# Kernel tuning notes

Measured on AMD Instinct MI355X. Metric: run time of the kernel, lower is better.

Reference implementation:

```python
import jax, jax.numpy as jnp
import numpy as np
from jax import lax

DIM = 64           # LHMSA dim
C3 = 3 * DIM       # high-band channels
HEADS = C3 // 32   # 6
WS = 8             # window size
SHIFT = 4          # shift size
EPS = 1e-6


def _ln_chw(x, w, b):
    # channel-last layer norm applied to BCHW input over C
    xt = x.transpose(0, 2, 3, 1)
    mu = xt.mean(-1, keepdims=True)
    var = ((xt - mu) ** 2).mean(-1, keepdims=True)
    y = (xt - mu) / jnp.sqrt(var + EPS) * w + b
    return y.transpose(0, 3, 1, 2)


def _conv1x1(x, w):
    # w: (out_c, in_c), no bias
    return jnp.einsum('bchw,oc->bohw', x, w)


def _dwconv3(x, w):
    # depthwise 3x3, w: (C,1,3,3)
    C = x.shape[1]
    return lax.conv_general_dilated(x, w, (1, 1), ((1, 1), (1, 1)),
                                    dimension_numbers=('NCHW', 'OIHW', 'NCHW'),
                                    feature_group_count=C)


def _gelu(x):
    return jax.nn.gelu(x, approximate=False)


def _dwt(x):
    x01 = x[:, :, 0::2, :] * 0.5
    x02 = x[:, :, 1::2, :] * 0.5
    x1 = x01[:, :, :, 0::2]; x2 = x02[:, :, :, 0::2]
    x3 = x01[:, :, :, 1::2]; x4 = x02[:, :, :, 1::2]
    ll = x1 + x2 + x3 + x4
    high = jnp.concatenate([-x1 - x2 + x3 + x4,
                            -x1 + x2 - x3 + x4,
                            x1 - x2 - x3 + x4], axis=1)
    return ll, high


def _iwt(ll, high):
    B, C, H, W = ll.shape
    hl, lh, hh = jnp.split(high, 3, axis=1)
    x1 = (ll - hl - lh + hh) * 0.5
    x2 = (ll - hl + lh - hh) * 0.5
    x3 = (ll + hl - lh - hh) * 0.5
    x4 = (ll + hl + lh + hh) * 0.5
    even = jnp.stack([x1, x3], axis=-1).reshape(B, C, H, 2 * W)  # rows 0::2
    odd = jnp.stack([x2, x4], axis=-1).reshape(B, C, H, 2 * W)   # rows 1::2
    return jnp.stack([even, odd], axis=-2).reshape(B, C, 2 * H, 2 * W)


def _swin_mhsa(x, qkv_w, qkv_b, proj_w, proj_b, rpb_table, rpi):
    # x: (B, C3, H, W); H,W divisible by WS -> no padding path
    B, C, H, W = x.shape
    dh = C // HEADS
    scale = dh ** (-0.5)
    xh = x.transpose(0, 2, 3, 1)                           # BHWC
    xh = jnp.roll(xh, (-SHIFT, -SHIFT), axis=(1, 2))
    nh, nw = H // WS, W // WS
    xw = xh.reshape(B, nh, WS, nw, WS, C).transpose(0, 1, 3, 2, 4, 5)
    xw = xw.reshape(B * nh * nw, WS * WS, C)               # (nW, N, C)
    qkv = xw @ qkv_w.T + qkv_b                             # (nW, N, 3C)
    qkv = qkv.reshape(-1, WS * WS, 3, HEADS, dh).transpose(2, 0, 3, 1, 4)
    q, k, v = qkv[0], qkv[1], qkv[2]                       # (nW, h, N, dh)
    attn = jnp.einsum('whnd,whmd->whnm', q, k) * scale
    bias = rpb_table[rpi.reshape(-1)].reshape(WS * WS, WS * WS, HEADS)
    attn = jax.nn.softmax(attn + bias.transpose(2, 0, 1)[None], axis=-1)
    out = jnp.einsum('whnm,whmd->whnd', attn, v)
    out = out.transpose(0, 2, 1, 3).reshape(-1, WS * WS, C)
    out = out.reshape(B, nh, nw, WS, WS, C).transpose(0, 1, 3, 2, 4, 5)
    out = out.reshape(B, H, W, C)
    out = jnp.roll(out, (SHIFT, SHIFT), axis=(1, 2))
    out = out @ proj_w.T + proj_b
    return out.transpose(0, 3, 1, 2)


def _rel_pos_index():
    coords = np.stack(np.meshgrid(np.arange(WS), np.arange(WS), indexing='ij'))
    cf = coords.reshape(2, -1)
    rel = (cf[:, :, None] - cf[:, None, :]).transpose(1, 2, 0).astype(np.int64)
    rel[:, :, 0] += WS - 1
    rel[:, :, 1] += WS - 1
    rel[:, :, 0] *= 2 * WS - 1
    return rel.sum(-1)


def setup_inputs() -> dict:
    key = jax.random.key(0)
    ks = jax.random.split(key, 12)
    B, H, W = 2, 512, 512
    x = jax.random.normal(ks[0], (B, DIM, H, W), jnp.float32)
    s = 0.02
    inp = {
        'x': x,
        'norm_w': jnp.ones((C3,), jnp.float32),
        'norm_b': jnp.zeros((C3,), jnp.float32),
        'qkv_w': jax.random.normal(ks[1], (3 * C3, C3), jnp.float32) * s,
        'qkv_b': jnp.zeros((3 * C3,), jnp.float32),
        'proj_w': jax.random.normal(ks[2], (C3, C3), jnp.float32) * s,
        'proj_b': jnp.zeros((C3,), jnp.float32),
        'rpb_table': jax.random.normal(ks[3], ((2 * WS - 1) ** 2, HEADS), jnp.float32) * s,
        'aux_dw_w': jax.random.normal(ks[4], (DIM, 1, 3, 3), jnp.float32) * 0.1,
        'aux_pw_w': jax.random.normal(ks[5], (DIM, DIM), jnp.float32) * s,
        'cg1_w': jax.random.normal(ks[6], (C3 * 3 // 12, DIM), jnp.float32) * s,
        'cg2_w': jax.random.normal(ks[7], (C3, C3 * 3 // 12), jnp.float32) * s,
        'po_w': jax.random.normal(ks[8], (DIM, DIM), jnp.float32) * s,
        'gamma_main': jnp.full((1,), 1e-4, jnp.float32),
        'gamma_aux': jnp.full((1,), 0.5, jnp.float32),
        'gamma_cross': jnp.full((1,), 1e-5, jnp.float32),
        'rel_pos_index': jnp.asarray(_rel_pos_index(), jnp.int32),
    }
    return inp


def reference(x, norm_w, norm_b, qkv_w, qkv_b, proj_w, proj_b, rpb_table,
              aux_dw_w, aux_pw_w, cg1_w, cg2_w, po_w,
              gamma_main, gamma_aux, gamma_cross, rel_pos_index):
    ll, high = _dwt(x)
    high_norm = _ln_chw(high, norm_w, norm_b)
    refined_high = high + gamma_main * _swin_mhsa(high_norm, qkv_w, qkv_b,
                                                  proj_w, proj_b, rpb_table,
                                                  rel_pos_index)
    refined_ll = ll + gamma_aux * _conv1x1(_gelu(_dwconv3(ll, aux_dw_w)), aux_pw_w)
    gap = ll.mean((2, 3), keepdims=True)
    cross = jax.nn.sigmoid(_conv1x1(_gelu(_conv1x1(gap, cg1_w)), cg2_w))
    refined_high = refined_high * (1.0 + gamma_cross * (cross - 0.5) * 2.0)
    out = _iwt(refined_ll, refined_high)
    return _conv1x1(out - x, po_w)
```

## Files before the change

kernel.cpp:

```cpp
#include <hip/hip_runtime.h>
#include <hip/hip_bf16.h>
#include <math.h>

typedef __hip_bfloat16 bf16;
typedef short s8v __attribute__((ext_vector_type(8)));
typedef float f4v __attribute__((ext_vector_type(4)));
#define MFMA16(a,b,c) __builtin_amdgcn_mfma_f32_16x16x32_bf16(a,b,c,0,0,0)

#define B2   2
#define C64  64
#define C3   192
#define HEADS 6
#define NWIN 2048

#define P_NORMW 0
#define P_NORMB 192
#define P_QKVW  384
#define P_QKVB  110976
#define P_PROJW 111552
#define P_PROJB 148416
#define P_RPB   148608
#define P_AUXDW 149958
#define P_AUXPW 150534
#define P_CG1   154630
#define P_CG2   157702
#define P_PO    166918
#define P_GM    171014
#define P_GA    171015
#define P_GC    171016

#define WS_FLAG   0
#define WS_PARAMS 256
#define WS_GAP    684544
#define WS_TSTAT  689664
#define WS_LL     1738240
#define WS_DLLW   18515456
#define WS_WOUT   35292672
#define WS_HRAW   85624320
#define WS_WQKV   135955968
#define WS_WPROJ  136177152
#define WS_WPW    136250880
#define WS_WPO    136259072
#define WS_S12    136267264
#define WS_BIAS6  136271872

__device__ __forceinline__ float bfu(unsigned short u){
  return __uint_as_float(((unsigned)u) << 16);
}
__device__ __forceinline__ float LDR(const void* p, long i, bool isf){
  return isf ? ((const float*)p)[i] : bfu(((const unsigned short*)p)[i]);
}
template<bool ISF>
__device__ __forceinline__ float4 LD4(const void* p, long i){
  if constexpr (ISF) return *(const float4*)((const float*)p + i);
  else {
    const ushort4 u = *(const ushort4*)((const bf16*)p + i);
    float4 r; r.x = bfu(u.x); r.y = bfu(u.y); r.z = bfu(u.z); r.w = bfu(u.w);
    return r;
  }
}
template<bool ISF>
__device__ __forceinline__ void ST(void* p, long i, float v){
  if constexpr (ISF) ((float*)p)[i] = v;
  else ((bf16*)p)[i] = __float2bfloat16(v);
}
__device__ __forceinline__ float gelu_f(float x){
  const float z = 0.7978845608028654f * (x + 0.044715f * x*x*x);
  const float t = 1.f - 2.f / (__expf(2.f*z) + 1.f);
  return 0.5f * x * (1.f + t);
}
__device__ __forceinline__ unsigned pk2(float a, float b){
  return (unsigned)__bfloat16_as_ushort(__float2bfloat16(a)) |
         ((unsigned)__bfloat16_as_ushort(__float2bfloat16(b)) << 16);
}
__device__ __forceinline__ uint4 pk8(const float* v){
  uint4 r;
  r.x = pk2(v[0], v[1]); r.y = pk2(v[2], v[3]);
  r.z = pk2(v[4], v[5]); r.w = pk2(v[6], v[7]);
  return r;
}
__device__ __forceinline__ void gld16(const void* g, void* l){
  __builtin_amdgcn_global_load_lds(
      (const __attribute__((address_space(1))) void*)g,
      (__attribute__((address_space(3))) void*)l, 16, 0, 0);
}

__global__ __launch_bounds__(256) void detect_kernel(const void* x, int* flag){
  __shared__ int wildcnt;
  if (threadIdx.x == 0) wildcnt = 0;
  __syncthreads();
  const unsigned short* u = (const unsigned short*)x;
  int wild = 0;
  for (int i = threadIdx.x; i < 2048; i += 256){
    unsigned int v = ((unsigned int)u[i]) << 16;
    float f = __uint_as_float(v);
    float a = fabsf(f);
    if (!(a < 1e8f) || (a > 0.f && a < 1e-8f)) wild++;
  }
  atomicAdd(&wildcnt, wild);
  __syncthreads();
  if (threadIdx.x == 0) *flag = (wildcnt > 100) ? 1 : 0;
}

struct PP { const void* src[15]; float* dst[15]; int n[15]; };
__device__ void kprep_body(int vblk, const PP& pp, bool isf, const int* rpi,
                           bf16* wqkvF, bf16* wproj, bf16* wpw,
                           bf16* wpo, float* bias6T, float2* s12p){
  const int gid = vblk*256 + threadIdx.x;
  const int gsz = 512*256;
#pragma unroll
  for (int q = 0; q < 15; q++){
    const int n = pp.n[q];
    const void* s = pp.src[q];
    float* d = pp.dst[q];
    for (int i = gid; i < n; i += gsz) d[i] = LDR(s, i, isf);
  }
  const void* qkvw = pp.src[2];
  const void* normw = pp.src[0];
  for (int i = gid; i < 110592; i += gsz)
    wqkvF[i] = __float2bfloat16(LDR(qkvw, i, isf) * LDR(normw, i % 192, isf));
  for (int i = gid; i < 36864; i += gsz)
    wproj[i] = __float2bfloat16(LDR(pp.src[4], i, isf));
  for (int i = gid; i < 4096; i += gsz){
    wpw[i] = __float2bfloat16(LDR(pp.src[8], i, isf));
    wpo[i] = __float2bfloat16(LDR(pp.src[11], i, isf));
  }
  for (int j = gid; j < 24576; j += gsz){
    const int hh = j >> 12, nm = j & 4095;
    const int row = nm >> 6, col = nm & 63;
    bias6T[hh*4096 + col*64 + row] = LDR(pp.src[6], rpi[nm]*6 + hh, isf);
  }
  const int o = gid >> 4, lane = gid & 15;
  if (o < 576){
    float s1 = 0.f, s2 = 0.f;
    for (int c = lane; c < 192; c += 16){
      const float w = LDR(qkvw, o*192 + c, isf);
      s1 += w * LDR(normw, c, isf);
      s2 += w * LDR(pp.src[1], c, isf);
    }
    s1 += __shfl_xor(s1,1,16); s1 += __shfl_xor(s1,2,16);
    s1 += __shfl_xor(s1,4,16); s1 += __shfl_xor(s1,8,16);
    s2 += __shfl_xor(s2,1,16); s2 += __shfl_xor(s2,2,16);
    s2 += __shfl_xor(s2,4,16); s2 += __shfl_xor(s2,8,16);
    if (lane == 0){
      float2 v; v.x = s1; v.y = s2 + LDR(pp.src[3], o, isf);
      s12p[o] = v;
    }
  }
}

template<bool ISF>
__device__ void k1f_body(int wid, const void* xv, bf16* llb, bf16* hraw, float2* tstat){
  const int b  = wid >> 10;
  const int wh = (wid >> 5) & 31;
  const int ww = wid & 31;
  const int tid = threadIdx.x;
  const int tp = tid >> 3, l8 = tid & 7;
  const int t0 = tp*2;
  const int wi = t0 >> 3, wj0 = t0 & 7;
  const int h2 = (wh*8 + wi + 4) & 255;
  const int w2 = (ww*8 + wj0 + 4) & 255;
  const long rowbase = ((long)(2*h2) << 9) + 2*w2;
  float r0[3][8], r1[3][8];
  float s0 = 0.f, q0 = 0.f, s1 = 0.f, q1 = 0.f;
#pragma unroll
  for (int g4 = 0; g4 < 2; ++g4){
    float4 ta[4], tb[4];
#pragma unroll
    for (int u = 0; u < 4; ++u){
      const int c = l8*8 + g4*4 + u;
      const long base = ((long)(b*64 + c) << 18) + rowbase;
      ta[u] = LD4<ISF>(xv, base);
      tb[u] = LD4<ISF>(xv, base + 512);
    }
#pragma unroll
    for (int u = 0; u < 4; ++u){
      const int cc = g4*4 + u;
      const int c = l8*8 + cc;
      float a = ta[u].x, cr = ta[u].y, bb = tb[u].x, dd = tb[u].y;
      const float ll0 = 0.5f*(a + bb + cr + dd);
      const float h00 = 0.5f*(-a - bb + cr + dd);
      const float h10 = 0.5f*(-a + bb - cr + dd);
      const float h20 = 0.5f*( a - bb - cr + dd);
      r0[0][cc] = h00; r0[1][cc] = h10; r0[2][cc] = h20;
      s0 += h00 + h10 + h20; q0 += h00*h00 + h10*h10 + h20*h20;
      a = ta[u].z; cr = ta[u].w; bb = tb[u].z; dd = tb[u].w;
      const float ll1 = 0.5f*(a + bb + cr + dd);
      const float h01 = 0.5f*(-a - bb + cr + dd);
      const float h11 = 0.5f*(-a + bb - cr + dd);
      const float h21 = 0.5f*( a - bb - cr + dd);
      r1[0][cc] = h01; r1[1][cc] = h11; r1[2][cc] = h21;
      s1 += h01 + h11 + h21; q1 += h01*h01 + h11*h11 + h21*h21;
      *(unsigned*)(llb + ((long)(b*64 + c) << 16) + ((long)h2 << 8) + w2) = pk2(ll0, ll1);
    }
  }
  const long hb = ((long)wid*64 + t0)*192 + l8*8;
  *(uint4*)(hraw + hb)            = pk8(r0[0]);
  *(uint4*)(hraw + hb + 64)       = pk8(r0[1]);
  *(uint4*)(hraw + hb + 128)      = pk8(r0[2]);
  *(uint4*)(hraw + hb + 192)      = pk8(r1[0]);
  *(uint4*)(hraw + hb + 192 + 64) = pk8(r1[1]);
  *(uint4*)(hraw + hb + 192 +128) = pk8(r1[2]);
  s0 += __shfl_xor(s0,1,8); s0 += __shfl_xor(s0,2,8); s0 += __shfl_xor(s0,4,8);
  q0 += __shfl_xor(q0,1,8); q0 += __shfl_xor(q0,2,8); q0 += __shfl_xor(q0,4,8);
  s1 += __shfl_xor(s1,1,8); s1 += __shfl_xor(s1,2,8); s1 += __shfl_xor(s1,4,8);
  q1 += __shfl_xor(q1,1,8); q1 += __shfl_xor(q1,2,8); q1 += __shfl_xor(q1,4,8);
  if (l8 == 0){
    float mean = s0 * (1.f/192.f);
    float var = fmaxf(q0 * (1.f/192.f) - mean*mean, 0.f);
    float rstd = rsqrtf(var + 1e-6f);
    float2 st; st.x = rstd; st.y = mean * rstd;
    tstat[wid*64 + t0] = st;
    mean = s1 * (1.f/192.f);
    var = fmaxf(q1 * (1.f/192.f) - mean*mean, 0.f);
    rstd = rsqrtf(var + 1e-6f);
    st.x = rstd; st.y = mean * rstd;
    tstat[wid*64 + t0 + 1] = st;
  }
}

__global__ __launch_bounds__(256,4) void k1p(const void* xv, bf16* llb, bf16* hraw,
                                             float2* tstat, const int* flag, PP pp,
                                             const int* rpi, bf16* wqkvF, bf16* wproj,
                                             bf16* wpw, bf16* wpo, float* bias6T,
                                             float2* s12p){
  const bool isf = (*flag) != 0;
  const int blk = blockIdx.x;
  if (blk < NWIN){
    if (isf) k1f_body<true>(blk, xv, llb, hraw, tstat);
    else     k1f_body<false>(blk, xv, llb, hraw, tstat);
  } else {
    kprep_body(blk - NWIN, pp, isf, rpi, wqkvF, wproj, wpw, wpo, bias6T, s12p);
  }
}

__device__ void k4_body(char* sm, int g, const bf16* hraw, const float2* tstat,
                        const bf16* wqkvF, const float2* s12p, const float* bias6T,
                        bf16* wout){
  bf16* bstage = (bf16*)sm;
  const int xcd = g & 7, slot = g >> 3;
  const int pair = (slot/6)*8 + xcd;
  const int h    = slot - (slot/6)*6;
  const int tid = threadIdx.x;
  const int wv5 = tid >> 6;
  const int lw  = wv5 >> 2;
  const int rg  = wv5 & 3;
  const int l = tid & 63, lr = l & 15, lg = l >> 4;
  const int wid = pair*2 + lw;
  char* reg = sm + 36864 + lw*13312;
  bf16* bq = (bf16*)reg;
  bf16* bk = (bf16*)(reg + 4608);
  char* vtb = reg + 9216;
  bf16* bp = (bf16*)reg;
  const f4v fz = {0.f,0.f,0.f,0.f};
  const float scale = 0.17677669529663687f;
  const bf16* at = hraw + (long)wid * 12288;

#pragma unroll
  for (int pass = 0; pass < 5; ++pass){
    if (pass*512 + wv5*64 < 2304){
      const int idx = pass*512 + tid;
      const int rl  = idx / 24;
      const int off = (idx - rl*24) * 16;
      const int soff = off ^ ((rl & 7) << 4);
      const int grow = (rl >> 5)*192 + h*32 + (rl & 31);
      gld16(wqkvF + grow*192 + (soff >> 1),
            (char*)bstage + (pass*512 + wv5*64)*16);
    }
  }
  s8v aA[6];
#pragma unroll
  for (int ks = 0; ks < 6; ++ks)
    aA[ks] = *(const s8v*)(at + (rg*16+lr)*192 + ks*32 + lg*8);
  float2 st4[4];
#pragma unroll
  for (int i = 0; i < 4; ++i)
    st4[i] = tstat[wid*64 + rg*16 + lg*4 + i];
  __syncthreads();

  f4v acc[6];
#pragma unroll
  for (int nt = 0; nt < 6; ++nt) acc[nt] = fz;
  __builtin_amdgcn_s_setprio(1);
#pragma unroll
  for (int ks = 0; ks < 6; ++ks){
    const int kb = (ks*32 + lg*8) * 2;
#pragma unroll
    for (int nt = 0; nt < 6; ++nt){
      const int row = nt*16 + lr;
      const s8v bfr = *(const s8v*)((const char*)bstage + row*384 + (kb ^ ((row&7)<<4)));
      acc[nt] = MFMA16(aA[ks], bfr, acc[nt]);
    }
  }
  __builtin_amdgcn_s_setprio(0);
#pragma unroll
  for (int nt = 0; nt < 6; ++nt){
    const int ol = nt*16 + lr;
    const int p = ol >> 5, c = ol & 31;
    const int ocol = p*192 + h*32 + c;
    const float2 sp = s12p[ocol];
#pragma unroll
    for (int i = 0; i < 4; ++i){
      const int row = rg*16 + lg*4 + i;
      const float v = st4[i].x*acc[nt][i] - st4[i].y*sp.x + sp.y;
      if (p == 0)      bq[row*36 + c] = __float2bfloat16(v*scale);
      else if (p == 1) bk[row*36 + c] = __float2bfloat16(v);
      else             *(bf16*)(vtb + ((c*128 + row*2) ^ ((c&7)<<4))) = __float2bfloat16(v);
    }
  }
  __syncthreads();

  f4v bld[4];
#pragma unroll
  for (int nt = 0; nt < 4; ++nt)
    bld[nt] = *(const f4v*)(bias6T + h*4096 + (nt*16+lr)*64 + rg*16 + lg*4);
  f4v sacc[4];
  {
    const s8v a = *(const s8v*)(bq + (rg*16+lr)*36 + lg*8);
#pragma unroll
    for (int nt = 0; nt < 4; ++nt){
      const s8v bfr = *(const s8v*)(bk + (nt*16+lr)*36 + lg*8);
      sacc[nt] = MFMA16(a, bfr, bld[nt]);
    }
  }
  float pvv[4][4];
  float inv4[4];
#pragma unroll
  for (int i = 0; i < 4; ++i){
    float s = 0.f;
#pragma unroll
    for (int nt = 0; nt < 4; ++nt){
      const float e = __expf(sacc[nt][i]);
      pvv[i][nt] = e;
      s += e;
    }
    s += __shfl_xor(s, 1, 16);
    s += __shfl_xor(s, 2, 16);
    s += __shfl_xor(s, 4, 16);
    s += __shfl_xor(s, 8, 16);
    inv4[i] = 1.f/s;
  }
  __syncthreads();

#pragma unroll
  for (int i = 0; i < 4; ++i){
    const int row = rg*16 + lg*4 + i;
#pragma unroll
    for (int nt = 0; nt < 4; ++nt)
      bp[row*72 + nt*16 + lr] = __float2bfloat16(pvv[i][nt]);
  }
  f4v oacc[2] = {fz, fz};
  __builtin_amdgcn_s_setprio(1);
#pragma unroll
  for (int ks2 = 0; ks2 < 2; ++ks2){
    const s8v a = *(const s8v*)(bp + (rg*16+lr)*72 + ks2*32 + lg*8);
#pragma unroll
    for (int nn = 0; nn < 2; ++nn){
      const int d = nn*16 + lr;
      const s8v bfr = *(const s8v*)(vtb + ((d*128 + (ks2*32+lg*8)*2) ^ ((d&7)<<4)));
      oacc[nn] = MFMA16(a, bfr, oacc[nn]);
    }
  }
  __builtin_amdgcn_s_setprio(0);
#pragma unroll
  for (int nn = 0; nn < 2; ++nn)
#pragma unroll
    for (int i = 0; i < 4; ++i){
      const int row = rg*16 + lg*4 + i;
      wout[((long)wid*64 + row)*192 + h*32 + nn*16 + lr] =
        __float2bfloat16(oacc[nn][i] * inv4[i]);
    }
}

__device__ void k6f_body(char* smb, int blk6, const bf16* llb, const float* pf,
                         const bf16* wpw, bf16* dllw){
  const int tid = threadIdx.x;
  const int sub = tid >> 8;
  const int t2 = tid & 255;
  char* sm6 = smb + sub*24576;
  bf16* tile = (bf16*)sm6;
  bf16* t    = (bf16*)(sm6 + 15360);
  const int tl = blk6*2 + sub;
  const int b = tl >> 10, ti = (tl >> 5) & 31, tj = tl & 31;
  const int y0 = ti*8 - 1;
  const int x0 = tj*8 - 2;

  for (int e = t2; e < 7680; e += 256){
    const int col = e % 12;
    const int rc  = e / 12;
    const int row = rc % 10, ch = rc / 10;
    const int x = x0 + col, y = y0 + row;
    bf16 v = __float2bfloat16(0.f);
    if ((unsigned)x < 256u && (unsigned)y < 256u)
      v = llb[((long)(b*64 + ch) << 16) + ((long)y << 8) + x];
    tile[rc*12 + col] = v;
  }
  __syncthreads();

  {
    const int tok = t2 & 63, cgrp = t2 >> 6;
    const int iy = tok >> 3, ix = tok & 7;
#pragma unroll
    for (int cc = 0; cc < 16; ++cc){
      const int c = cgrp*16 + cc;
      const float* wk = pf + P_AUXDW + c*9;
      float s = 0.f;
#pragma unroll
      for (int ky = 0; ky < 3; ++ky)
#pragma unroll
        for (int kx = 0; kx < 3; ++kx)
          s += wk[ky*3 + kx] * __bfloat162float(tile[(c*10 + iy + ky)*12 + ix + 1 + kx]);
      t[tok*72 + c] = __float2bfloat16(gelu_f(s));
    }
  }
  __syncthreads();

  const int wv = t2 >> 6, l = t2 & 63, lr = l & 15, lg = l >> 4;
  const f4v fz = {0.f,0.f,0.f,0.f};
  f4v acc[4];
#pragma unroll
  for (int nt = 0; nt < 4; ++nt) acc[nt] = fz;
#pragma unroll
  for (int ks = 0; ks < 2; ++ks){
    const s8v a = *(const s8v*)(t + (wv*16+lr)*72 + ks*32 + lg*8);
#pragma unroll
    for (int nt = 0; nt < 4; ++nt){
      const s8v bfr = *(const s8v*)(wpw + (nt*16+lr)*64 + ks*32 + lg*8);
      acc[nt] = MFMA16(a, bfr, acc[nt]);
    }
  }
  const float ga = pf[P_GA];
#pragma unroll
  for (int i = 0; i < 4; ++i){
    const int p = wv*16 + lg*4 + i;
    const int y = ti*8 + (p >> 3), x = tj*8 + (p & 7);
    const int sy = (y - 4) & 255, sx = (x - 4) & 255;
    const int wd = b*1024 + (sy >> 3)*32 + (sx >> 3);
    const int tok2 = (sy & 7)*8 + (sx & 7);
    const long ob = ((long)wd*64 + tok2)*64;
#pragma unroll
    for (int nt = 0; nt < 4; ++nt)
      dllw[ob + nt*16 + lr] = __float2bfloat16(ga * acc[nt][i]);
  }
}

__device__ void k2_body(char* smb, int bc, const bf16* llb, float* gap){
  float* red = (float*)smb;
  const int tid = threadIdx.x;
  const uint4* p = (const uint4*)(llb + ((long)bc << 16));
  float s = 0.f;
  for (int i = tid; i < 8192; i += 512){
    const uint4 v = p[i];
    s += __uint_as_float(v.x << 16) + __uint_as_float(v.x & 0xffff0000u);
    s += __uint_as_float(v.y << 16) + __uint_as_float(v.y & 0xffff0000u);
    s += __uint_as_float(v.z << 16) + __uint_as_float(v.z & 0xffff0000u);
    s += __uint_as_float(v.w << 16) + __uint_as_float(v.w & 0xffff0000u);
  }
  red[tid] = s; __syncthreads();
  for (int st = 256; st > 0; st >>= 1){
    if (tid < st) red[tid] += red[tid + st];
    __syncthreads();
  }
  if (tid == 0) gap[bc] = red[0] * (1.f / 65536.f);
}

__global__ __launch_bounds__(512,4) void kmix(const bf16* hraw, const float2* tstat,
                                              const bf16* wqkvF, const float2* s12p,
                                              const float* bias6T, bf16* wout,
                                              const bf16* llb, const float* pf,
                                              const bf16* wpw, bf16* dllw, float* gap){
  __shared__ __align__(16) char sm[63488];
  const int blk = blockIdx.x;
  if (blk < 7168){
    const int g7 = blk / 7, r7 = blk - g7*7;
    if (r7 < 6) k4_body(sm, g7*6 + r7, hraw, tstat, wqkvF, s12p, bias6T, wout);
    else        k6f_body(sm, g7, llb, pf, wpw, dllw);
  } else {
    k2_body(sm, blk - 7168, llb, gap);
  }
}

__global__ __launch_bounds__(256,5) void k5_proj(bf16* wout, const bf16* hraw,
                                                 const bf16* wproj, const float* pf,
                                                 const float* gap){
  __shared__ __align__(16) bf16 bufC[64*192];
  __shared__ float t1s[48];
  __shared__ float amL[192], cvL[192];
  const int wid = blockIdx.x;
  const int b  = wid >> 10;
  const int tid = threadIdx.x;
  const int wv = tid >> 6, l = tid & 63, lr = l & 15, lg = l >> 4;

  {
    const bf16* hsrc = hraw + (long)wid * 12288;
#pragma unroll
    for (int pass = 0; pass < 6; ++pass){
      const int idx = pass*256 + tid;
      const int row = idx / 24;
      const int off = (idx % 24) * 16;
      const int soff = off ^ ((row & 7) << 4);
      gld16(hsrc + row*192 + (soff >> 1),
            (char*)bufC + (pass*256 + wv*64)*16);
    }
  }

  if (tid < 48){
    float s = 0.f;
    const float* w = pf + P_CG1 + tid*64;
    for (int c = 0; c < 64; ++c) s += w[c] * gap[b*64 + c];
    t1s[tid] = gelu_f(s);
  }
  __syncthreads();
  if (tid < 192){
    float s = 0.f;
    const float* w = pf + P_CG2 + tid*48;
    for (int j = 0; j < 48; ++j) s += w[j] * t1s[j];
    const float cr = 1.f / (1.f + __expf(-s));
    const float cc = pf[P_GC] * (cr - 0.5f) * 2.f;
    cvL[tid] = cc;
    amL[tid] = pf[P_GM] * (1.f + cc);
  }

  const f4v fz = {0.f,0.f,0.f,0.f};
  const bf16* at = wout + (long)wid * 12288;

  f4v acc[3][4];
#pragma unroll
  for (int nt = 0; nt < 3; ++nt)
#pragma unroll
    for (int mt = 0; mt < 4; ++mt) acc[nt][mt] = fz;
#pragma unroll
  for (int ks = 0; ks < 6; ++ks){
    const int k0 = ks*32;
    s8v a[4];
#pragma unroll
    for (int mt = 0; mt < 4; ++mt)
      a[mt] = *(const s8v*)(at + (mt*16+lr)*192 + k0 + lg*8);
#pragma unroll
    for (int nt = 0; nt < 3; ++nt){
      const int ocol = (wv*3+nt)*16 + lr;
      const s8v bfr = *(const s8v*)(wproj + ocol*192 + k0 + lg*8);
#pragma unroll
      for (int mt = 0; mt < 4; ++mt) acc[nt][mt] = MFMA16(a[mt], bfr, acc[nt][mt]);
    }
  }
  __syncthreads();
#pragma unroll
  for (int nt = 0; nt < 3; ++nt){
    const int col = (wv*3+nt)*16 + lr;
    const float am = amL[col], cv = cvL[col], pb = pf[P_PROJB + col];
#pragma unroll
    for (int mt = 0; mt < 4; ++mt)
#pragma unroll
      for (int i = 0; i < 4; ++i){
        const int row = mt*16 + lg*4 + i;
        const float hv = __bfloat162float(
          *(const bf16*)((const char*)bufC + row*384 + ((col*2) ^ ((row&7)<<4))));
        wout[(long)wid*12288 + row*192 + col] =
          __float2bfloat16(am*(acc[nt][mt][i] + pb) + cv*hv);
      }
  }
}

template<bool ISF>
__device__ void k7_body(const bf16* dvalw, const bf16* dllw, const bf16* wpo,
                        void* out, char* yp){
  const int blk = blockIdx.x;
  const int b = blk >> 10, hh = (blk >> 1) & 511, half = blk & 1;
  const int h2 = hh >> 1, posH = hh & 1;
  const int th = (h2 + 252) & 255;
  const int wh = th >> 3, wi = th & 7;
  const int tid = threadIdx.x;
  const int j = tid & 7;
#pragma unroll
  for (int pass = 0; pass < 8; ++pass){
    const int p = pass*32 + (tid >> 3);
    const int ww2 = half*256 + p;
    const int w2 = ww2 >> 1, posW = ww2 & 1;
    const int tw = (w2 + 252) & 255;
    const int ww = tw >> 3, wj = tw & 7;
    const int wid = b*1024 + wh*32 + ww;
    const int tok = wi*8 + wj;
    const long dvb = ((long)wid*64 + tok)*192 + j*8;
    const s8v hl8 = *(const s8v*)(dvalw + dvb);
    const s8v lh8 = *(const s8v*)(dvalw + dvb + 64);
    const s8v hh8 = *(const s8v*)(dvalw + dvb + 128);
    const s8v dl8 = *(const s8v*)(dllw + ((long)wid*64 + tok)*64 + j*8);
    const float s1 = posW ? 0.5f : -0.5f;
    const float s2 = posH ? 0.5f : -0.5f;
    const float s3 = posW == posH ? 0.5f : -0.5f;
    float e[8];
#pragma unroll
    for (int q = 0; q < 8; ++q)
      e[q] = 0.5f*bfu((unsigned short)dl8[q]) + s1*bfu((unsigned short)hl8[q])
           + s2*bfu((unsigned short)lh8[q]) + s3*bfu((unsigned short)hh8[q]);
    *(uint4*)(yp + ((p*128 + j*16) ^ ((p&7)<<4))) = pk8(e);
  }
  __syncthreads();
  const int wv = tid >> 6, l = tid & 63, lr = l & 15, lg = l >> 4;
  const f4v fz = {0.f,0.f,0.f,0.f};
  f4v acc[4][4];
#pragma unroll
  for (int mt = 0; mt < 4; ++mt)
#pragma unroll
    for (int nt = 0; nt < 4; ++nt) acc[mt][nt] = fz;
#pragma unroll
  for (int ks = 0; ks < 2; ++ks){
    const int k0 = ks*32;
    s8v a[4];
#pragma unroll
    for (int mt = 0; mt < 4; ++mt)
      a[mt] = *(const s8v*)(wpo + (mt*16+lr)*64 + k0 + lg*8);
#pragma unroll
    for (int nt = 0; nt < 4; ++nt){
      const int prow = wv*64 + nt*16 + lr;
      const s8v bfr = *(const s8v*)(yp + ((prow*128 + (k0+lg*8)*2) ^ ((prow&7)<<4)));
#pragma unroll
      for (int mt = 0; mt < 4; ++mt) acc[mt][nt] = MFMA16(a[mt], bfr, acc[mt][nt]);
    }
  }
  const int px0 = half*256 + wv*64;
#pragma unroll
  for (int mt = 0; mt < 4; ++mt)
#pragma unroll
    for (int nt = 0; nt < 4; ++nt)
#pragma unroll
      for (int i = 0; i < 4; ++i){
        const int c = mt*16 + lg*4 + i;
        const long ob = ((long)(b*64 + c)*512 + hh)*512 + px0 + nt*16 + lr;
        ST<ISF>(out, ob, acc[mt][nt][i]);
      }
}
__global__ __launch_bounds__(256,4) void k7_out(const bf16* dvalw, const bf16* dllw,
                                                const bf16* wpo, void* out, const int* flag){
  __shared__ __align__(16) char yp[32768];
  if (*flag) k7_body<true>(dvalw, dllw, wpo, out, yp);
  else       k7_body<false>(dvalw, dllw, wpo, out, yp);
}

extern "C" void kernel_launch(void* const* d_in, const int* in_sizes, int n_in,
                              void* d_out, int out_size, void* d_ws, size_t ws_size,
                              hipStream_t stream){
  char* ws = (char*)d_ws;
  int*   flag = (int*)(ws + WS_FLAG);
  float* pf   = (float*)(ws + WS_PARAMS);
  float* gap  = (float*)(ws + WS_GAP);
  float2* tstat=(float2*)(ws + WS_TSTAT);
  bf16*  llb  = (bf16*)(ws + WS_LL);
  bf16*  dllw = (bf16*)(ws + WS_DLLW);
  bf16*  wout = (bf16*)(ws + WS_WOUT);
  bf16*  hraw = (bf16*)(ws + WS_HRAW);
  bf16*  wqkvF= (bf16*)(ws + WS_WQKV);
  bf16*  wproj= (bf16*)(ws + WS_WPROJ);
  bf16*  wpw  = (bf16*)(ws + WS_WPW);
  bf16*  wpo  = (bf16*)(ws + WS_WPO);
  float2* s12p= (float2*)(ws + WS_S12);
  float* bias6= (float*)(ws + WS_BIAS6);
  const int* rpi = (const int*)d_in[16];

  detect_kernel<<<1, 256, 0, stream>>>(d_in[0], flag);

  PP pp;
  const int pidx[15] = {1,2,3,4,5,6,7,8,9,10,11,12,13,14,15};
  const int poff[15] = {P_NORMW,P_NORMB,P_QKVW,P_QKVB,P_PROJW,P_PROJB,P_RPB,
                        P_AUXDW,P_AUXPW,P_CG1,P_CG2,P_PO,P_GM,P_GA,P_GC};
  for (int q = 0; q < 15; q++){
    pp.src[q] = d_in[pidx[q]];
    pp.dst[q] = pf + poff[q];
    pp.n[q]   = in_sizes[pidx[q]];
  }

  k1p    <<<NWIN + 512, 256, 0, stream>>>(d_in[0], llb, hraw, tstat, flag, pp, rpi,
                                          wqkvF, wproj, wpw, wpo, bias6, s12p);
  kmix   <<<7296, 512, 0, stream>>>(hraw, tstat, wqkvF, s12p, bias6, wout,
                                    llb, pf, wpw, dllw, gap);
  k5_proj<<<NWIN, 256, 0, stream>>>(wout, hraw, wproj, pf, gap);
  k7_out <<<2048, 256, 0, stream>>>(wout, dllw, wpo, d_out, flag);
}
```

Before: 380.1 us.

## Pre-swizzle QKV weights into MFMA fragment order and load directly from global

The prep kernel now writes the norm-folded QKV weight in the exact per-lane MFMA B-fragment order, so the attention body reads each fragment with one 16-byte global load instead of staging 36 KB through LDS. This removes the LDS staging pass, a block barrier, and 15 KB of shared memory per block, which can allow more resident blocks. It also drops the s_setprio hints. The risk is that every wave now pulls its weight fragments from L2/global, with more redundant traffic and latency exposed inside the MFMA loop.

```diff
diff --git a/kernel.cpp b/kernel.cpp
--- a/kernel.cpp
+++ b/kernel.cpp
@@ -43,6 +43,7 @@
 #define WS_WPO    136259072
 #define WS_S12    136267264
 #define WS_BIAS6  136271872
+#define WS_WQKVR  136370176
 
 __device__ __forceinline__ float bfu(unsigned short u){
   return __uint_as_float(((unsigned)u) << 16);
@@ -104,7 +105,7 @@
 
 struct PP { const void* src[15]; float* dst[15]; int n[15]; };
 __device__ void kprep_body(int vblk, const PP& pp, bool isf, const int* rpi,
-                           bf16* wqkvF, bf16* wproj, bf16* wpw,
+                           bf16* wqkvR, bf16* wproj, bf16* wpw,
                            bf16* wpo, float* bias6T, float2* s12p){
   const int gid = vblk*256 + threadIdx.x;
   const int gsz = 512*256;
@@ -117,8 +118,19 @@
   }
   const void* qkvw = pp.src[2];
   const void* normw = pp.src[0];
-  for (int i = gid; i < 110592; i += gsz)
-    wqkvF[i] = __float2bfloat16(LDR(qkvw, i, isf) * LDR(normw, i % 192, isf));
+  for (int i = gid; i < 110592; i += gsz){
+    const int e  = i & 7;
+    const int l  = (i >> 3) & 63;
+    const int nt = (i >> 9) % 6;
+    const int ks = (i >> 9) / 6 % 6;
+    const int h  = (i >> 9) / 36;
+    const int lr = l & 15, lg = l >> 4;
+    const int ol = nt*16 + lr;
+    const int p = ol >> 5, c = ol & 31;
+    const int ocol = p*192 + h*32 + c;
+    const int k = ks*32 + lg*8 + e;
+    wqkvR[i] = __float2bfloat16(LDR(qkvw, ocol*192 + k, isf) * LDR(normw, k, isf));
+  }
   for (int i = gid; i < 36864; i += gsz)
     wproj[i] = __float2bfloat16(LDR(pp.src[4], i, isf));
   for (int i = gid; i < 4096; i += gsz){
@@ -221,7 +233,7 @@
 
 __global__ __launch_bounds__(256,4) void k1p(const void* xv, bf16* llb, bf16* hraw,
                                              float2* tstat, const int* flag, PP pp,
-                                             const int* rpi, bf16* wqkvF, bf16* wproj,
+                                             const int* rpi, bf16* wqkvR, bf16* wproj,
                                              bf16* wpw, bf16* wpo, float* bias6T,
                                              float2* s12p){
   const bool isf = (*flag) != 0;
@@ -230,14 +242,13 @@
     if (isf) k1f_body<true>(blk, xv, llb, hraw, tstat);
     else     k1f_body<false>(blk, xv, llb, hraw, tstat);
   } else {
-    kprep_body(blk - NWIN, pp, isf, rpi, wqkvF, wproj, wpw, wpo, bias6T, s12p);
+    kprep_body(blk - NWIN, pp, isf, rpi, wqkvR, wproj, wpw, wpo, bias6T, s12p);
   }
 }
 
 __device__ void k4_body(char* sm, int g, const bf16* hraw, const float2* tstat,
-                        const bf16* wqkvF, const float2* s12p, const float* bias6T,
+                        const bf16* wqkvR, const float2* s12p, const float* bias6T,
                         bf16* wout){
-  bf16* bstage = (bf16*)sm;
   const int xcd = g & 7, slot = g >> 3;
   const int pair = (slot/6)*8 + xcd;
   const int h    = slot - (slot/6)*6;
@@ -247,7 +258,7 @@
   const int rg  = wv5 & 3;
   const int l = tid & 63, lr = l & 15, lg = l >> 4;
   const int wid = pair*2 + lw;
-  char* reg = sm + 36864 + lw*13312;
+  char* reg = sm + lw*13312;
   bf16* bq = (bf16*)reg;
   bf16* bk = (bf16*)(reg + 4608);
   char* vtb = reg + 9216;
@@ -255,19 +266,8 @@
   const f4v fz = {0.f,0.f,0.f,0.f};
   const float scale = 0.17677669529663687f;
   const bf16* at = hraw + (long)wid * 12288;
-
-#pragma unroll
-  for (int pass = 0; pass < 5; ++pass){
-    if (pass*512 + wv5*64 < 2304){
-      const int idx = pass*512 + tid;
-      const int rl  = idx / 24;
-      const int off = (idx - rl*24) * 16;
-      const int soff = off ^ ((rl & 7) << 4);
-      const int grow = (rl >> 5)*192 + h*32 + (rl & 31);
-      gld16(wqkvF + grow*192 + (soff >> 1),
-            (char*)bstage + (pass*512 + wv5*64)*16);
-    }
-  }
+  const bf16* wR = wqkvR + (long)h*18432 + (l << 3);
+
   s8v aA[6];
 #pragma unroll
   for (int ks = 0; ks < 6; ++ks)
@@ -276,23 +276,18 @@
 #pragma unroll
   for (int i = 0; i < 4; ++i)
     st4[i] = tstat[wid*64 + rg*16 + lg*4 + i];
-  __syncthreads();
 
   f4v acc[6];
 #pragma unroll
   for (int nt = 0; nt < 6; ++nt) acc[nt] = fz;
-  __builtin_amdgcn_s_setprio(1);
 #pragma unroll
   for (int ks = 0; ks < 6; ++ks){
-    const int kb = (ks*32 + lg*8) * 2;
 #pragma unroll
     for (int nt = 0; nt < 6; ++nt){
-      const int row = nt*16 + lr;
-      const s8v bfr = *(const s8v*)((const char*)bstage + row*384 + (kb ^ ((row&7)<<4)));
+      const s8v bfr = *(const s8v*)(wR + (ks*6 + nt)*512);
       acc[nt] = MFMA16(aA[ks], bfr, acc[nt]);
     }
   }
-  __builtin_amdgcn_s_setprio(0);
 #pragma unroll
   for (int nt = 0; nt < 6; ++nt){
     const int ol = nt*16 + lr;
@@ -350,7 +345,6 @@
       bp[row*72 + nt*16 + lr] = __float2bfloat16(pvv[i][nt]);
   }
   f4v oacc[2] = {fz, fz};
-  __builtin_amdgcn_s_setprio(1);
 #pragma unroll
   for (int ks2 = 0; ks2 < 2; ++ks2){
     const s8v a = *(const s8v*)(bp + (rg*16+lr)*72 + ks2*32 + lg*8);
@@ -361,7 +355,6 @@
       oacc[nn] = MFMA16(a, bfr, oacc[nn]);
     }
   }
-  __builtin_amdgcn_s_setprio(0);
 #pragma unroll
   for (int nn = 0; nn < 2; ++nn)
 #pragma unroll
@@ -465,15 +458,15 @@
 }
 
 __global__ __launch_bounds__(512,4) void kmix(const bf16* hraw, const float2* tstat,
-                                              const bf16* wqkvF, const float2* s12p,
+                                              const bf16* wqkvR, const float2* s12p,
                                               const float* bias6T, bf16* wout,
                                               const bf16* llb, const float* pf,
                                               const bf16* wpw, bf16* dllw, float* gap){
-  __shared__ __align__(16) char sm[63488];
+  __shared__ __align__(16) char sm[49152];
   const int blk = blockIdx.x;
   if (blk < 7168){
     const int g7 = blk / 7, r7 = blk - g7*7;
-    if (r7 < 6) k4_body(sm, g7*6 + r7, hraw, tstat, wqkvF, s12p, bias6T, wout);
+    if (r7 < 6) k4_body(sm, g7*6 + r7, hraw, tstat, wqkvR, s12p, bias6T, wout);
     else        k6f_body(sm, g7, llb, pf, wpw, dllw);
   } else {
     k2_body(sm, blk - 7168, llb, gap);
@@ -650,12 +643,12 @@
   bf16*  dllw = (bf16*)(ws + WS_DLLW);
   bf16*  wout = (bf16*)(ws + WS_WOUT);
   bf16*  hraw = (bf16*)(ws + WS_HRAW);
-  bf16*  wqkvF= (bf16*)(ws + WS_WQKV);
   bf16*  wproj= (bf16*)(ws + WS_WPROJ);
   bf16*  wpw  = (bf16*)(ws + WS_WPW);
   bf16*  wpo  = (bf16*)(ws + WS_WPO);
   float2* s12p= (float2*)(ws + WS_S12);
   float* bias6= (float*)(ws + WS_BIAS6);
+  bf16*  wqkvR= (bf16*)(ws + WS_WQKVR);
   const int* rpi = (const int*)d_in[16];
 
   detect_kernel<<<1, 256, 0, stream>>>(d_in[0], flag);
@@ -671,8 +664,8 @@
   }
 
   k1p    <<<NWIN + 512, 256, 0, stream>>>(d_in[0], llb, hraw, tstat, flag, pp, rpi,
-                                          wqkvF, wproj, wpw, wpo, bias6, s12p);
-  kmix   <<<7296, 512, 0, stream>>>(hraw, tstat, wqkvF, s12p, bias6, wout,
+                                          wqkvR, wproj, wpw, wpo, bias6, s12p);
+  kmix   <<<7296, 512, 0, stream>>>(hraw, tstat, wqkvR, s12p, bias6, wout,
                                     llb, pf, wpw, dllw, gap);
   k5_proj<<<NWIN, 256, 0, stream>>>(wout, hraw, wproj, pf, gap);
   k7_out <<<2048, 256, 0, stream>>>(wout, dllw, wpo, d_out, flag);
```

Result: slower. 397.4 us (+4.6%).
